# Kernel optimization log

Hardware: AMD Instinct MI355X
Metric: run time of the kernel (lower is better)

The kernel has to match this reference:

```python
import jax, jax.numpy as jnp
import numpy as np

SCALE = 0.0625      # spatial_scale
OUT = 7             # out_size (== part_size)
C_OUT = 256         # output_dim (== input channels, group_size=1)
SPP = 4             # sample_per_part
TRANS_STD = 0.1
FC_DIM = 1024
B, H, W = 4, 128, 128
N_ROI = 2000
IMG = 2048.0        # H / SCALE


def _round_half(x):
    # CUDA round(): half away from zero (coords are non-negative here)
    return jnp.floor(x + 0.5)


def deform_roi_pool(data, rois, offset):
    """Faithful port of deform_roi_pooling (DCNv2 deform PS-ROI pooling, group_size=1).
    data: [B,C,H,W]; rois: [N,5]; offset: None or [N,2,OUT,OUT]. Returns [N,C,OUT,OUT]."""
    Bn, C, Hh, Ww = data.shape
    N = rois.shape[0]
    b = rois[:, 0].astype(jnp.int32)
    sw = _round_half(rois[:, 1]) * SCALE - 0.5
    sh = _round_half(rois[:, 2]) * SCALE - 0.5
    ew = (_round_half(rois[:, 3]) + 1.0) * SCALE - 0.5
    eh = (_round_half(rois[:, 4]) + 1.0) * SCALE - 0.5
    rw = jnp.maximum(ew - sw, 0.1)
    rh = jnp.maximum(eh - sh, 0.1)
    bw, bh = rw / OUT, rh / OUT              # bin sizes
    subw, subh = bw / SPP, bh / SPP          # sub-bin sizes

    ph, pw = jnp.meshgrid(jnp.arange(OUT, dtype=data.dtype),
                          jnp.arange(OUT, dtype=data.dtype), indexing='ij')
    wstart = pw[None] * bw[:, None, None] + sw[:, None, None]   # [N,OUT,OUT]
    hstart = ph[None] * bh[:, None, None] + sh[:, None, None]
    if offset is not None:
        # part_size == out_size -> part index == bin index
        wstart = wstart + offset[:, 0] * TRANS_STD * rw[:, None, None]
        hstart = hstart + offset[:, 1] * TRANS_STD * rh[:, None, None]

    ih2, iw2 = jnp.meshgrid(jnp.arange(SPP, dtype=data.dtype),
                            jnp.arange(SPP, dtype=data.dtype), indexing='ij')
    ih2, iw2 = ih2.reshape(-1), iw2.reshape(-1)  # [SPP*SPP]
    # sample coords [S2, N, OUT, OUT]
    ws = wstart[None] + iw2[:, None, None, None] * subw[None, :, None, None]
    hs = hstart[None] + ih2[:, None, None, None] * subh[None, :, None, None]

    bb = b[:, None, None]  # [N,1,1]

    def body(carry, coords):
        acc, cnt = carry
        w, h = coords                                 # [N,OUT,OUT]
        valid = (w >= -0.5) & (w <= Ww - 0.5) & (h >= -0.5) & (h <= Hh - 0.5)
        wc = jnp.clip(w, 0.0, Ww - 1.0)
        hc = jnp.clip(h, 0.0, Hh - 1.0)
        x0 = jnp.floor(wc).astype(jnp.int32)
        y0 = jnp.floor(hc).astype(jnp.int32)
        x1 = jnp.minimum(x0 + 1, Ww - 1)
        y1 = jnp.minimum(y0 + 1, Hh - 1)
        dx = wc - x0
        dy = hc - y0
        v00 = data[bb, :, y0, x0]   # [N,OUT,OUT,C]
        v01 = data[bb, :, y0, x1]
        v10 = data[bb, :, y1, x0]
        v11 = data[bb, :, y1, x1]
        val = (((1 - dx) * (1 - dy))[..., None] * v00
               + (dx * (1 - dy))[..., None] * v01
               + ((1 - dx) * dy)[..., None] * v10
               + (dx * dy)[..., None] * v11)
        val = jnp.where(valid[..., None], val, 0.0)
        return (acc + val, cnt + valid.astype(data.dtype)), None

    init = (jnp.zeros((N, OUT, OUT, C), data.dtype),
            jnp.zeros((N, OUT, OUT), data.dtype))
    (s, cnt), _ = jax.lax.scan(body, init, (ws, hs))
    out = jnp.where(cnt[..., None] > 0, s / jnp.maximum(cnt, 1.0)[..., None], 0.0)
    return jnp.transpose(out, (0, 3, 1, 2))  # [N,C,OUT,OUT]


def setup_inputs() -> dict:
    key = jax.random.key(0)
    ks = jax.random.split(key, 16)
    data = jax.random.normal(ks[0], (B, C_OUT, H, W), dtype=jnp.float32)
    bidx = jax.random.randint(ks[1], (N_ROI,), 0, B).astype(jnp.float32)
    x1 = jax.random.uniform(ks[2], (N_ROI,), minval=0.0, maxval=IMG - 64.0)
    y1 = jax.random.uniform(ks[3], (N_ROI,), minval=0.0, maxval=IMG - 64.0)
    wbox = jax.random.uniform(ks[4], (N_ROI,), minval=16.0, maxval=400.0)
    hbox = jax.random.uniform(ks[5], (N_ROI,), minval=16.0, maxval=400.0)
    rois = jnp.stack([bidx, x1, y1,
                      jnp.minimum(x1 + wbox, IMG - 1.0),
                      jnp.minimum(y1 + hbox, IMG - 1.0)], axis=1)
    fin = OUT * OUT * C_OUT  # 12544
    def lin(k, i, o, s=None):
        s = (1.0 / np.sqrt(i)) if s is None else s
        return jax.random.normal(k, (i, o), dtype=jnp.float32) * s
    return {
        'data': data, 'rois': rois,
        'w1': lin(ks[6], fin, FC_DIM), 'b1': jnp.zeros((FC_DIM,), jnp.float32),
        'w2': lin(ks[7], FC_DIM, FC_DIM), 'b2': jnp.zeros((FC_DIM,), jnp.float32),
        'w3': lin(ks[8], FC_DIM, OUT * OUT * 2, 0.01), 'b3': jnp.zeros((OUT * OUT * 2,), jnp.float32),
        'mw1': lin(ks[9], fin, FC_DIM), 'mb1': jnp.zeros((FC_DIM,), jnp.float32),
        'mw2': lin(ks[10], FC_DIM, OUT * OUT, 0.01), 'mb2': jnp.zeros((OUT * OUT,), jnp.float32),
    }


def reference(data, rois, w1, b1, w2, b2, w3, b3, mw1, mb1, mw2, mb2):
    n = rois.shape[0]
    x = deform_roi_pool(data, rois, None)              # [N,C,OUT,OUT]
    xf = x.reshape(n, -1)
    h = jax.nn.relu(xf @ w1 + b1)
    h = jax.nn.relu(h @ w2 + b2)
    offset = (h @ w3 + b3).reshape(n, 2, OUT, OUT)
    m = jax.nn.relu(xf @ mw1 + mb1)
    mask = jax.nn.sigmoid(m @ mw2 + mb2).reshape(n, 1, OUT, OUT)
    feat = deform_roi_pool(data, rois, offset) * mask
    return feat
```

## Files before the change

### kernel.cpp

```cpp
#include <hip/hip_runtime.h>
#include <math.h>

#define WDIM 128
#define HDIM 128
#define BDIM 4
#define CDIM 256
#define NROI 2000
#define MPAD 2048
#define FIN  12544
#define FC   1024
#define HWC  (HDIM * WDIM * CDIM)

typedef unsigned short bf16r;
typedef unsigned short u16;
typedef __attribute__((ext_vector_type(8))) short bf16x8;
typedef __attribute__((ext_vector_type(4))) float f32x4;
typedef __attribute__((ext_vector_type(8))) _Float16 half8;
typedef __attribute__((ext_vector_type(8))) unsigned short ushort8v;

__device__ __forceinline__ bf16r f2bf(float f) {
    unsigned u = __float_as_uint(f);
    u += 0x7FFFu + ((u >> 16) & 1u);
    return (bf16r)(u >> 16);
}
__device__ __forceinline__ u16 f2h(float f) {
    union { u16 s; _Float16 h; } c; c.h = (_Float16)f; return c.s;
}

__device__ __forceinline__ void async16(const bf16r* g, bf16r* l) {
    __builtin_amdgcn_global_load_lds(
        (const __attribute__((address_space(1))) unsigned int*)g,
        (__attribute__((address_space(3))) unsigned int*)l, 16, 0, 0);
}

#define VMW(n) asm volatile("s_waitcnt vmcnt(" #n ")" ::: "memory")
#define BARRIER() __builtin_amdgcn_s_barrier()

__device__ __forceinline__ void roi_geom(const float* __restrict__ rois, int n,
                                         int& b, float& sw, float& sh,
                                         float& rw, float& rh) {
    const float* r = rois + (size_t)n * 5;
    b = (int)r[0];
    float r1 = floorf(r[1] + 0.5f);
    float r2 = floorf(r[2] + 0.5f);
    float r3 = floorf(r[3] + 0.5f);
    float r4 = floorf(r[4] + 0.5f);
    sw = r1 * 0.0625f - 0.5f;
    sh = r2 * 0.0625f - 0.5f;
    float ew = (r3 + 1.0f) * 0.0625f - 0.5f;
    float eh = (r4 + 1.0f) * 0.0625f - 0.5f;
    rw = fmaxf(ew - sw, 0.1f);
    rh = fmaxf(eh - sh, 0.1f);
}

__device__ __forceinline__ void build_geometry(
        int n, int tid, const float* __restrict__ rois,
        const float* __restrict__ offs,
        const float* __restrict__ maskb,
        float* axW, unsigned* axMeta, uint2* wpix, int* npx, float* scale) {
    if (tid < 98) {
        int po = tid >> 1, axis = tid & 1;
        int b; float sw, sh, rw, rh;
        roi_geom(rois, n, b, sw, sh, rw, rh);
        float bw = rw * (1.f / 7.f), bh = rh * (1.f / 7.f);
        int ph = po / 7, pw = po - ph * 7;
        float start, sub;
        if (axis == 0) {
            start = (float)pw * bw + sw;
            if (offs) start += offs[(size_t)n * 98 + po] * 0.1f * rw;
            sub = bw * 0.25f;
        } else {
            start = (float)ph * bh + sh;
            if (offs) start += offs[(size_t)n * 98 + 49 + po] * 0.1f * rh;
            sub = bh * 0.25f;
        }
        float wsl[5] = {0.f, 0.f, 0.f, 0.f, 0.f};
        int base = 0, cnt = 0, mx = 0, any = 0;
#pragma unroll
        for (int i = 0; i < 4; ++i) {
            float p = start + (float)i * sub;
            bool valid = (p >= -0.5f) & (p <= 127.5f);
            float pc = fminf(fmaxf(p, 0.f), 127.f);
            int p0 = (int)floorf(pc);
            float d = pc - (float)p0;
            int p1 = min(p0 + 1, 127);
            if (valid) {
                if (!any) { base = p0; any = 1; }
                int c0 = p0 - base, c1 = p1 - base;
                float w0 = 1.f - d;
#pragma unroll
                for (int k = 0; k < 5; ++k)
                    wsl[k] += ((c0 == k) ? w0 : 0.f) + ((c1 == k) ? d : 0.f);
                cnt++;
                mx = max(mx, c1);
            }
        }
        int N = any ? mx + 1 : 0;
        axMeta[tid] = (unsigned)(N | (cnt << 3) | (base << 6));
#pragma unroll
        for (int k = 0; k < 5; ++k) axW[tid * 5 + k] = wsl[k];
    }
    __syncthreads();
    if (tid < 245) {
        int po = tid / 5, r = tid - po * 5;
        unsigned mx_ = axMeta[po * 2], my_ = axMeta[po * 2 + 1];
        int NX = mx_ & 7, NY = my_ & 7;
        int bx = (mx_ >> 6) & 127, by = (my_ >> 6) & 127;
        if (r == 0) {
            int cntx = (mx_ >> 3) & 7, cnty = (my_ >> 3) & 7;
            int ct = cntx * cnty;
            float sc = (ct > 0) ? 1.f / (float)ct : 0.f;
            if (maskb) sc *= (ct > 0) ? maskb[(size_t)n * 49 + po] : 0.f;
            npx[po] = NX * NY;
            scale[po] = sc;
        }
        if (r < NY) {
            float wyr = axW[(po * 2 + 1) * 5 + r];
            unsigned rowoff = (unsigned)(((by + r) * 128 + bx) * 512);
#pragma unroll
            for (int c = 0; c < 5; ++c)
                if (c < NX)
                    wpix[po * 28 + r * NX + c] =
                        make_uint2(rowoff + (unsigned)c * 512u,
                                   __float_as_uint(wyr * axW[po * 2 * 5 + c]));
        }
    }
    __syncthreads();
}

__global__ __launch_bounds__(256) void transpose_kernel(const float* __restrict__ data,
                                                        u16* __restrict__ data_t) {
    __shared__ float t[32][33];
    int x0 = blockIdx.x << 5;
    int c0 = blockIdx.y << 5;
    int b  = blockIdx.z >> 7;
    int y  = blockIdx.z & 127;
    int tx = threadIdx.x, ty = threadIdx.y;
#pragma unroll
    for (int i = 0; i < 32; i += 8)
        t[ty + i][tx] = data[(((size_t)b * CDIM + c0 + ty + i) * HDIM + y) * WDIM + x0 + tx];
    __syncthreads();
#pragma unroll
    for (int i = 0; i < 32; i += 8)
        data_t[(((size_t)b * HDIM + y) * WDIM + x0 + ty + i) * CDIM + c0 + tx] = f2h(t[tx][ty + i]);
}

__global__ __launch_bounds__(256) void conv_kernel(const float* __restrict__ srcA,
                                                   const float* __restrict__ srcB,
                                                   int nsplit, int ncols, int Nout,
                                                   int K, int perm,
                                                   bf16r* __restrict__ dst) {
    __shared__ float t[32][33];
    int k0 = blockIdx.x << 5, n0 = blockIdx.y << 5;
    int tx = threadIdx.x & 31, ty = threadIdx.x >> 5;
#pragma unroll
    for (int i = 0; i < 32; i += 8) {
        int k = k0 + ty + i;
        int n = n0 + tx;
        const float* s = (n < nsplit) ? srcA : srcB;
        int col = (n < nsplit) ? n : n - nsplit;
        int row = perm ? ((k & 255) * 49 + (k >> 8)) : k;
        float v = (n < Nout && col < ncols) ? s[(size_t)row * ncols + col] : 0.f;
        t[ty + i][tx] = v;
    }
    __syncthreads();
#pragma unroll
    for (int i = 0; i < 32; i += 8) {
        int n = n0 + ty + i;
        if (n < Nout) dst[(size_t)n * K + k0 + tx] = f2bf(t[tx][ty + i]);
    }
}

__global__ __launch_bounds__(512) void pool1_kernel(const u16* __restrict__ data_t,
                                                    const float* __restrict__ rois,
                                                    bf16r* __restrict__ xf) {
    __shared__ ushort tileX[49][264];
    __shared__ float axW[98 * 5];
    __shared__ unsigned axMeta[98];
    __shared__ uint2 wpix[49 * 28];
    __shared__ int npx[49];
    __shared__ float scale[49];
    int n = blockIdx.x, tid = threadIdx.x;
    build_geometry(n, tid, rois, nullptr, nullptr, axW, axMeta, wpix, npx, scale);
    int b = (int)rois[(size_t)n * 5];
    int wave = tid >> 6, lane = tid & 63, shalf = lane >> 5, c8 = (lane & 31) << 3;
    const char* dpb = (const char*)(data_t + (size_t)b * HWC + c8);
    for (int po = wave * 2 + shalf; po < 49; po += 16) {
        int npe = npx[po];
        float sc = scale[po];
        const uint2* wp = wpix + po * 28;
        float a[8];
#pragma unroll
        for (int k = 0; k < 8; ++k) a[k] = 0.f;
        int p = 0;
        for (; p + 2 <= npe; p += 2) {
            uint2 q0 = wp[p], q1 = wp[p + 1];
            half8 v0 = *(const half8*)(dpb + q0.x);
            half8 v1 = *(const half8*)(dpb + q1.x);
            float w0 = __uint_as_float(q0.y), w1 = __uint_as_float(q1.y);
#pragma unroll
            for (int k = 0; k < 8; ++k) a[k] += w0 * (float)v0[k];
#pragma unroll
            for (int k = 0; k < 8; ++k) a[k] += w1 * (float)v1[k];
        }
        if (p < npe) {
            uint2 q0 = wp[p];
            half8 v0 = *(const half8*)(dpb + q0.x);
            float w0 = __uint_as_float(q0.y);
#pragma unroll
            for (int k = 0; k < 8; ++k) a[k] += w0 * (float)v0[k];
        }
        ushort8v o;
#pragma unroll
        for (int k = 0; k < 8; ++k) o[k] = f2bf(a[k] * sc);
        *(ushort8v*)&tileX[po][c8] = o;
    }
    __syncthreads();
    bf16r* xp = xf + (size_t)n * FIN;
    for (int u = tid; u < 3136; u += 512) {
        int k0 = u << 2;
        ushort4 o;
#pragma unroll
        for (int j = 0; j < 4; ++j) {
            int k = k0 + j;
            int c = k / 49;
            int po = k - c * 49;
            ((ushort*)&o)[j] = tileX[po][c];
        }
        *(ushort4*)(xp + k0) = o;
    }
}

__global__ __launch_bounds__(512) void pool2_kernel(const u16* __restrict__ data_t,
                                                    const float* __restrict__ rois,
                                                    const float* __restrict__ offs,
                                                    const float* __restrict__ maskb,
                                                    float* __restrict__ out) {
    __shared__ float tile[49 * 128];
    __shared__ float axW[98 * 5];
    __shared__ unsigned axMeta[98];
    __shared__ uint2 wpix[49 * 28];
    __shared__ int npx[49];
    __shared__ float scale[49];
    int n = blockIdx.x, chalf = blockIdx.y, tid = threadIdx.x;
    build_geometry(n, tid, rois, offs, maskb, axW, axMeta, wpix, npx, scale);
    int b = (int)rois[(size_t)n * 5];
    int wave = tid >> 6, lane = tid & 63, q = lane >> 4, c8 = (lane & 15) << 3;
    const char* dpb = (const char*)(data_t + (size_t)b * HWC + chalf * 128 + c8);
    for (int po = wave * 4 + q; po < 49; po += 32) {
        int npe = npx[po];
        float sc = scale[po];
        const uint2* wp = wpix + po * 28;
        float a[8];
#pragma unroll
        for (int k = 0; k < 8; ++k) a[k] = 0.f;
        int p = 0;
        for (; p + 2 <= npe; p += 2) {
            uint2 q0 = wp[p], q1 = wp[p + 1];
            half8 v0 = *(const half8*)(dpb + q0.x);
            half8 v1 = *(const half8*)(dpb + q1.x);
            float w0 = __uint_as_float(q0.y), w1 = __uint_as_float(q1.y);
#pragma unroll
            for (int k = 0; k < 8; ++k) a[k] += w0 * (float)v0[k];
#pragma unroll
            for (int k = 0; k < 8; ++k) a[k] += w1 * (float)v1[k];
        }
        if (p < npe) {
            uint2 q0 = wp[p];
            half8 v0 = *(const half8*)(dpb + q0.x);
            float w0 = __uint_as_float(q0.y);
#pragma unroll
            for (int k = 0; k < 8; ++k) a[k] += w0 * (float)v0[k];
        }
        int cs = c8 ^ ((po & 7) << 3);
        float4 lo = make_float4(a[0] * sc, a[1] * sc, a[2] * sc, a[3] * sc);
        float4 hi = make_float4(a[4] * sc, a[5] * sc, a[6] * sc, a[7] * sc);
        *(float4*)&tile[po * 128 + cs] = lo;
        *(float4*)&tile[po * 128 + cs + 4] = hi;
    }
    __syncthreads();
    float* op = out + (size_t)n * FIN + (size_t)chalf * 6272;
    for (int i = tid; i < 6272; i += 512) {
        int c = i / 49, po = i - c * 49;
        op[i] = tile[po * 128 + (c ^ ((po & 7) << 3))];
    }
}

#define STAGE_A(buf, h, kt) do { \
    async16(Abase + (size_t)(kt) * 64 + sAoff[h][0], &lds[buf][0][((h) * 128 + wave * 8) * 64]); \
    async16(Abase + (size_t)(kt) * 64 + sAoff[h][1], &lds[buf][0][((h) * 128 + 64 + wave * 8) * 64]); \
} while (0)
#define STAGE_B(buf, h, kt) do { \
    async16(Bbase + (size_t)(kt) * 64 + sBoff[h][0], &lds[buf][1][((h) * 128 + wave * 8) * 64]); \
    async16(Bbase + (size_t)(kt) * 64 + sBoff[h][1], &lds[buf][1][((h) * 128 + 64 + wave * 8) * 64]); \
} while (0)
#define LDA_HALF(buf, mh) do { \
    const char* Ar = (const char*)&lds[buf][0][0] + aQ + (mh) * 16384; \
    _Pragma("unroll") for (int i = 0; i < 4; ++i) \
        _Pragma("unroll") for (int ks = 0; ks < 2; ++ks) \
            aF[i][ks] = *(const bf16x8*)(Ar + i * 2048 + fRB[ks]); \
} while (0)
#define LDB_HALF(dst, buf, nh) do { \
    const char* Br = (const char*)&lds[buf][1][0] + bQ + (nh) * 16384; \
    _Pragma("unroll") for (int jf = 0; jf < 2; ++jf) \
        _Pragma("unroll") for (int ks = 0; ks < 2; ++ks) \
            dst[jf][ks] = *(const bf16x8*)(Br + jf * 2048 + fRB[ks]); \
} while (0)
#define MMA_Q(mh, nh, B) do { \
    __builtin_amdgcn_s_setprio(1); \
    _Pragma("unroll") for (int i = 0; i < 4; ++i) \
        _Pragma("unroll") for (int jf = 0; jf < 2; ++jf) \
            _Pragma("unroll") for (int ks = 0; ks < 2; ++ks) \
                acc[(mh) * 4 + i][(nh) * 2 + jf] = __builtin_amdgcn_mfma_f32_16x16x32_bf16( \
                    aF[i][ks], B[jf][ks], acc[(mh) * 4 + i][(nh) * 2 + jf], 0, 0, 0); \
    __builtin_amdgcn_s_setprio(0); \
} while (0)

__global__ __launch_bounds__(512, 2) void gemm256_kernel(
        const bf16r* __restrict__ A, int lda,
        const bf16r* __restrict__ Bt, int ldb,
        float* __restrict__ P, int Npad, int KS, int ktiles) {
    __shared__ bf16r lds[2][2][256 * 64];
    int tid = threadIdx.x;
    int wave = tid >> 6, lane = tid & 63;
    int l15 = lane & 15, quad = lane >> 4;
    int wm = wave >> 2, wn = wave & 3;

    int idx = blockIdx.x + gridDim.x * blockIdx.y;
    int nid = (idx & 7) * ((gridDim.x * gridDim.y) >> 3) + (idx >> 3);
    int bx = nid % gridDim.x, by = nid / gridDim.x;
    int m0 = by << 8, n0 = bx << 8;
    int z = blockIdx.z;

    int sAoff[2][2], sBoff[2][2];
#pragma unroll
    for (int h = 0; h < 2; ++h)
#pragma unroll
        for (int j = 0; j < 2; ++j) {
            int slot = h * 128 + j * 64 + wave * 8 + (lane >> 3);
            int g = (lane & 7) ^ ((slot >> 1) & 7);
            int rowA = ((slot >> 6) & 1) * 128 + (slot >> 7) * 64 + (slot & 63);
            int colB = ((slot >> 5) & 3) * 64 + (slot >> 7) * 32 + (slot & 31);
            sAoff[h][j] = rowA * lda + g * 8;
            sBoff[h][j] = colB * ldb + g * 8;
        }
    const bf16r* Abase = A + (size_t)m0 * lda;
    const bf16r* Bbase = Bt + (size_t)n0 * ldb;

    int fRB[2];
#pragma unroll
    for (int ks = 0; ks < 2; ++ks)
        fRB[ks] = l15 * 128 + ((((ks << 2) + quad) ^ ((l15 >> 1) & 7)) << 4);
    int aQ = wm * 8192;
    int bQ = wn * 4096;

    f32x4 acc[8][4];
#pragma unroll
    for (int i = 0; i < 8; ++i)
#pragma unroll
        for (int j = 0; j < 4; ++j) acc[i][j] = (f32x4){0.f, 0.f, 0.f, 0.f};
    bf16x8 aF[4][2], bF0[2][2], bF1[2][2];

    int tb = ((ktiles * z) / KS) & ~1;
    int te = (z == KS - 1) ? ktiles : ((ktiles * (z + 1)) / KS) & ~1;
    int nit = (te - tb) >> 1;

    STAGE_A(0, 0, tb); STAGE_B(0, 0, tb); STAGE_A(0, 1, tb); STAGE_B(0, 1, tb);
    STAGE_A(1, 0, tb + 1); STAGE_B(1, 0, tb + 1);
    VMW(4);
    BARRIER();

    for (int it = 0; it < nit; ++it) {
        int t1 = tb + 2 * it + 1, nx0 = t1 + 1, nx1 = t1 + 2;
        bool last = (it == nit - 1);
        LDA_HALF(0, 0); LDB_HALF(bF0, 0, 0);
        STAGE_A(1, 1, t1);
        BARRIER();
        MMA_Q(0, 0, bF0);
        BARRIER();

        LDB_HALF(bF1, 0, 1);
        STAGE_B(1, 1, t1);
        BARRIER();
        MMA_Q(0, 1, bF1);
        BARRIER();

        LDA_HALF(0, 1);
        if (!last) STAGE_A(0, 0, nx0);
        BARRIER();
        MMA_Q(1, 1, bF1);
        BARRIER();

        if (!last) STAGE_B(0, 0, nx0);
        BARRIER();
        MMA_Q(1, 0, bF0);
        if (last) { VMW(0); } else { VMW(4); }
        BARRIER();

        LDA_HALF(1, 0); LDB_HALF(bF0, 1, 0);
        if (!last) STAGE_A(0, 1, nx0);
        BARRIER();
        MMA_Q(0, 0, bF0);
        BARRIER();

        LDB_HALF(bF1, 1, 1);
        if (!last) STAGE_B(0, 1, nx0);
        BARRIER();
        MMA_Q(0, 1, bF1);
        BARRIER();

        LDA_HALF(1, 1);
        if (!last) STAGE_A(1, 0, nx1);
        BARRIER();
        MMA_Q(1, 1, bF1);
        BARRIER();

        if (!last) STAGE_B(1, 0, nx1);
        BARRIER();
        MMA_Q(1, 0, bF0);
        if (!last) { VMW(4); }
        BARRIER();
    }

    float* Pp = P + (size_t)z * MPAD * Npad;
#pragma unroll
    for (int I = 0; I < 8; ++I) {
        int row = m0 + wm * 128 + I * 16 + quad * 4;
#pragma unroll
        for (int J = 0; J < 4; ++J) {
            int col = n0 + wn * 64 + J * 16 + l15;
            float* o = Pp + (size_t)row * Npad + col;
#pragma unroll
            for (int r = 0; r < 4; ++r) o[(size_t)r * Npad] = acc[I][J][r];
        }
    }
}

__global__ __launch_bounds__(256) void gemm_mfma_kernel(
        const bf16r* __restrict__ A, int lda,
        const bf16r* __restrict__ Bt, int K,
        float* __restrict__ P, int Npad, int KS) {
    __shared__ bf16r As[128 * 32];
    __shared__ bf16r Bs[128 * 32];
    int tid = threadIdx.x;
    int wave = tid >> 6, lane = tid & 63;
    int nwgxy = gridDim.x * gridDim.y;
    int idx = blockIdx.x + gridDim.x * blockIdx.y;
    int chunk = nwgxy >> 3;
    int nid = (idx & 7) * chunk + (idx >> 3);
    int bx = nid % gridDim.x, by = nid / gridDim.x;
    int m0 = by << 7, n0 = bx << 7;
    int z = blockIdx.z;

    int srow = lane >> 2;
    int kchunk = ((lane & 3) ^ ((lane >> 3) & 3)) << 3;
    const bf16r* aG0 = A + (size_t)(m0 + wave * 32 + srow) * lda + kchunk;
    const bf16r* aG1 = A + (size_t)(m0 + wave * 32 + 16 + srow) * lda + kchunk;
    const bf16r* bG0 = Bt + (size_t)(n0 + wave * 32 + srow) * K + kchunk;
    const bf16r* bG1 = Bt + (size_t)(n0 + wave * 32 + 16 + srow) * K + kchunk;
    bf16r* aL0 = As + wave * 1024;
    bf16r* aL1 = As + wave * 1024 + 512;
    bf16r* bL0 = Bs + wave * 1024;
    bf16r* bL1 = Bs + wave * 1024 + 512;

    int l15 = lane & 15, quad = lane >> 4;
    int wr = wave >> 1, wc = wave & 1;
    int psw = (quad ^ ((l15 >> 1) & 3)) << 3;
    int aoff[4], boff[4];
#pragma unroll
    for (int t = 0; t < 4; ++t) {
        aoff[t] = ((wr * 64 + t * 16 + l15) * 32 + psw) * 2;
        boff[t] = ((wc * 64 + t * 16 + l15) * 32 + psw) * 2;
    }

    f32x4 acc[4][4];
#pragma unroll
    for (int i = 0; i < 4; ++i)
#pragma unroll
        for (int j = 0; j < 4; ++j) acc[i][j] = (f32x4){0.f, 0.f, 0.f, 0.f};

    int iters = K >> 5;
    int i0 = (int)((long)iters * z / KS);
    int i1 = (int)((long)iters * (z + 1) / KS);

    {
        size_t k0 = (size_t)i0 << 5;
        async16(aG0 + k0, aL0); async16(aG1 + k0, aL1);
        async16(bG0 + k0, bL0); async16(bG1 + k0, bL1);
    }
    for (int it = i0; it < i1; ++it) {
        __syncthreads();
        bf16x8 af[4], bfv[4];
#pragma unroll
        for (int t = 0; t < 4; ++t) af[t] = *(const bf16x8*)((const char*)As + aoff[t]);
#pragma unroll
        for (int t = 0; t < 4; ++t) bfv[t] = *(const bf16x8*)((const char*)Bs + boff[t]);
        __syncthreads();
        if (it + 1 < i1) {
            size_t k0 = (size_t)(it + 1) << 5;
            async16(aG0 + k0, aL0); async16(aG1 + k0, aL1);
            async16(bG0 + k0, bL0); async16(bG1 + k0, bL1);
        }
#pragma unroll
        for (int i = 0; i < 4; ++i)
#pragma unroll
            for (int j = 0; j < 4; ++j)
                acc[i][j] = __builtin_amdgcn_mfma_f32_16x16x32_bf16(af[i], bfv[j], acc[i][j], 0, 0, 0);
    }

    float* Pp = P + (size_t)z * MPAD * Npad;
#pragma unroll
    for (int i = 0; i < 4; ++i) {
        int row = m0 + wr * 64 + i * 16 + quad * 4;
#pragma unroll
        for (int j = 0; j < 4; ++j) {
            int col = n0 + wc * 64 + j * 16 + l15;
            float* o = Pp + (size_t)row * Npad + col;
#pragma unroll
            for (int r = 0; r < 4; ++r) o[(size_t)r * Npad] = acc[i][j][r];
        }
    }
}

__global__ __launch_bounds__(256) void reduce_kernel(
        const float* __restrict__ P, int shift, int KS,
        const float* __restrict__ bias0, const float* __restrict__ bias1, int bsplit,
        void* __restrict__ Out, int ldo, int M, int Nreal, int outmode) {
    int idx = (blockIdx.x * 256 + threadIdx.x) << 2;
    int Npad = 1 << shift;
    int row = idx >> shift, col = idx & (Npad - 1);
    f32x4 s = (f32x4){0.f, 0.f, 0.f, 0.f};
    size_t plane = (size_t)MPAD << shift;
    for (int zz = 0; zz < KS; ++zz) s += *(const f32x4*)(P + (size_t)zz * plane + idx);
    if (row < M) {
#pragma unroll
        for (int e = 0; e < 4; ++e) {
            int c = col + e;
            if (c < Nreal) {
                float b = (c < bsplit) ? bias0[c] : bias1[c - bsplit];
                float v = s[e] + b;
                if (outmode == 0) {
                    v = fmaxf(v, 0.f);
                    ((bf16r*)Out)[(size_t)row * ldo + c] = f2bf(v);
                } else {
                    if (outmode == 2) v = 1.f / (1.f + expf(-v));
                    ((float*)Out)[(size_t)row * ldo + c] = v;
                }
            }
        }
    }
}

extern "C" void kernel_launch(void* const* d_in, const int* in_sizes, int n_in,
                              void* d_out, int out_size, void* d_ws, size_t ws_size,
                              hipStream_t stream) {
    const float* data = (const float*)d_in[0];
    const float* rois = (const float*)d_in[1];
    const float* w1   = (const float*)d_in[2];
    const float* b1   = (const float*)d_in[3];
    const float* w2   = (const float*)d_in[4];
    const float* b2   = (const float*)d_in[5];
    const float* w3   = (const float*)d_in[6];
    const float* b3   = (const float*)d_in[7];
    const float* mw1  = (const float*)d_in[8];
    const float* mb1  = (const float*)d_in[9];
    const float* mw2  = (const float*)d_in[10];
    const float* mb2  = (const float*)d_in[11];
    float* out = (float*)d_out;

    char* w = (char*)d_ws;
    size_t off = 0;
    auto carve = [&](size_t bytes) {
        void* p = w + off;
        off += (bytes + 255) & ~(size_t)255;
        return p;
    };
    u16* data_t   = (u16*)carve((size_t)BDIM * HDIM * WDIM * CDIM * 2);
    bf16r* xf     = (bf16r*)carve((size_t)MPAD * FIN * 2);
    bf16r* bt1    = (bf16r*)carve((size_t)MPAD * FIN * 2);
    bf16r* hm     = (bf16r*)carve((size_t)MPAD * 2048 * 2);
    bf16r* h2     = (bf16r*)carve((size_t)MPAD * 1024 * 2);
    bf16r* bt2    = (bf16r*)carve((size_t)1024 * 1024 * 2);
    bf16r* bt3    = (bf16r*)carve((size_t)128 * 1024 * 2);
    bf16r* bt4    = (bf16r*)carve((size_t)128 * 1024 * 2);
    float* offs   = (float*)carve((size_t)NROI * 98 * 4);
    float* maskb  = (float*)carve((size_t)NROI * 49 * 4);
    float* P      = (float*)(w + off);
    size_t plane  = (size_t)MPAD * 2048 * 4;
    size_t avail  = (ws_size > off) ? ws_size - off : 0;
    int use256 = (avail >= 4 * plane);

    conv_kernel<<<dim3(392, 64), 256, 0, stream>>>(w1, mw1, 1024, 1024, 2048, FIN, 0, bt1);
    conv_kernel<<<dim3(32, 32), 256, 0, stream>>>(w2, w2, 1 << 30, 1024, 1024, 1024, 0, bt2);
    conv_kernel<<<dim3(32, 4), 256, 0, stream>>>(w3, w3, 1 << 30, 98, 98, 1024, 0, bt3);
    conv_kernel<<<dim3(32, 2), 256, 0, stream>>>(mw2, mw2, 1 << 30, 49, 49, 1024, 0, bt4);
    transpose_kernel<<<dim3(4, 8, 512), dim3(32, 8), 0, stream>>>(data, data_t);
    pool1_kernel<<<dim3(NROI), 512, 0, stream>>>(data_t, rois, xf);

    if (use256) {
        gemm256_kernel<<<dim3(8, 8, 4), 512, 0, stream>>>(xf, FIN, bt1, FIN, P, 2048, 4, 196);
        reduce_kernel<<<4096, 256, 0, stream>>>(P, 11, 4, b1, mb1, 1024, hm, 2048, NROI, 2048, 0);
        gemm256_kernel<<<dim3(4, 8, 8), 512, 0, stream>>>(hm, 2048, bt2, 1024, P, 1024, 8, 16);
        reduce_kernel<<<2048, 256, 0, stream>>>(P, 10, 8, b2, b2, 1 << 30, h2, 1024, NROI, 1024, 0);
    } else {
        gemm_mfma_kernel<<<dim3(16, 16, 3), 256, 0, stream>>>(xf, FIN, bt1, FIN, P, 2048, 3);
        reduce_kernel<<<4096, 256, 0, stream>>>(P, 11, 3, b1, mb1, 1024, hm, 2048, NROI, 2048, 0);
        gemm_mfma_kernel<<<dim3(8, 16, 4), 256, 0, stream>>>(hm, 2048, bt2, 1024, P, 1024, 4);
        reduce_kernel<<<2048, 256, 0, stream>>>(P, 10, 4, b2, b2, 1 << 30, h2, 1024, NROI, 1024, 0);
    }
    gemm_mfma_kernel<<<dim3(1, 16, 8), 256, 0, stream>>>(h2, 1024, bt3, 1024, P, 128, 8);
    reduce_kernel<<<256, 256, 0, stream>>>(P, 7, 8, b3, b3, 1 << 30, offs, 98, NROI, 98, 1);
    gemm_mfma_kernel<<<dim3(1, 16, 8), 256, 0, stream>>>(hm + 1024, 2048, bt4, 1024, P, 128, 8);
    reduce_kernel<<<256, 256, 0, stream>>>(P, 7, 8, mb2, mb2, 1 << 30, maskb, 49, NROI, 49, 2);

    pool2_kernel<<<dim3(NROI, 2), 512, 0, stream>>>(data_t, rois, offs, maskb, out);
}
```

Measured before the change: 526.9 us.

## Reorder ROI blocks by batch index and use 128-tile GEMM for second FC

Adds a single-block kernel that builds a remap of ROIs grouped by batch image. Both pooling kernels then process ROIs in that order, so blocks running at the same time read the same image plane and get better L2 reuse. The second FC layer now always uses the 128-tile MFMA GEMM with split-K of 4 instead of the 256-tile variant. The remap kernel adds one small serial launch, and its atomic ordering inside a batch is nondeterministic, though outputs are written by ROI index and stay correct.

```diff
diff --git a/kernel.cpp b/kernel.cpp
--- a/kernel.cpp
+++ b/kernel.cpp
@@ -51,6 +51,27 @@
     float eh = (r4 + 1.0f) * 0.0625f - 0.5f;
     rw = fmaxf(ew - sw, 0.1f);
     rh = fmaxf(eh - sh, 0.1f);
+}
+
+__global__ __launch_bounds__(256) void order_kernel(const float* __restrict__ rois,
+                                                    int* __restrict__ remap) {
+    __shared__ int cnt[4], base[4];
+    int tid = threadIdx.x;
+    if (tid < 4) cnt[tid] = 0;
+    __syncthreads();
+    for (int n = tid; n < NROI; n += 256)
+        atomicAdd(&cnt[(int)rois[(size_t)n * 5]], 1);
+    __syncthreads();
+    if (tid == 0) {
+        int s = 0;
+        for (int i = 0; i < 4; ++i) { base[i] = s; s += cnt[i]; cnt[i] = 0; }
+    }
+    __syncthreads();
+    for (int n = tid; n < NROI; n += 256) {
+        int b = (int)rois[(size_t)n * 5];
+        int pos = base[b] + atomicAdd(&cnt[b], 1);
+        remap[pos] = n;
+    }
 }
 
 __device__ __forceinline__ void build_geometry(
@@ -173,6 +194,7 @@
 
 __global__ __launch_bounds__(512) void pool1_kernel(const u16* __restrict__ data_t,
                                                     const float* __restrict__ rois,
+                                                    const int* __restrict__ remap,
                                                     bf16r* __restrict__ xf) {
     __shared__ ushort tileX[49][264];
     __shared__ float axW[98 * 5];
@@ -180,7 +202,7 @@
     __shared__ uint2 wpix[49 * 28];
     __shared__ int npx[49];
     __shared__ float scale[49];
-    int n = blockIdx.x, tid = threadIdx.x;
+    int n = remap[blockIdx.x], tid = threadIdx.x;
     build_geometry(n, tid, rois, nullptr, nullptr, axW, axMeta, wpix, npx, scale);
     int b = (int)rois[(size_t)n * 5];
     int wave = tid >> 6, lane = tid & 63, shalf = lane >> 5, c8 = (lane & 31) << 3;
@@ -233,6 +255,7 @@
 
 __global__ __launch_bounds__(512) void pool2_kernel(const u16* __restrict__ data_t,
                                                     const float* __restrict__ rois,
+                                                    const int* __restrict__ remap,
                                                     const float* __restrict__ offs,
                                                     const float* __restrict__ maskb,
                                                     float* __restrict__ out) {
@@ -242,7 +265,7 @@
     __shared__ uint2 wpix[49 * 28];
     __shared__ int npx[49];
     __shared__ float scale[49];
-    int n = blockIdx.x, chalf = blockIdx.y, tid = threadIdx.x;
+    int n = remap[blockIdx.x], chalf = blockIdx.y, tid = threadIdx.x;
     build_geometry(n, tid, rois, offs, maskb, axW, axMeta, wpix, npx, scale);
     int b = (int)rois[(size_t)n * 5];
     int wave = tid >> 6, lane = tid & 63, q = lane >> 4, c8 = (lane & 15) << 3;
@@ -585,33 +608,33 @@
     bf16r* bt4    = (bf16r*)carve((size_t)128 * 1024 * 2);
     float* offs   = (float*)carve((size_t)NROI * 98 * 4);
     float* maskb  = (float*)carve((size_t)NROI * 49 * 4);
+    int*   remap  = (int*)carve((size_t)NROI * 4);
     float* P      = (float*)(w + off);
     size_t plane  = (size_t)MPAD * 2048 * 4;
     size_t avail  = (ws_size > off) ? ws_size - off : 0;
     int use256 = (avail >= 4 * plane);
 
+    order_kernel<<<1, 256, 0, stream>>>(rois, remap);
     conv_kernel<<<dim3(392, 64), 256, 0, stream>>>(w1, mw1, 1024, 1024, 2048, FIN, 0, bt1);
     conv_kernel<<<dim3(32, 32), 256, 0, stream>>>(w2, w2, 1 << 30, 1024, 1024, 1024, 0, bt2);
     conv_kernel<<<dim3(32, 4), 256, 0, stream>>>(w3, w3, 1 << 30, 98, 98, 1024, 0, bt3);
     conv_kernel<<<dim3(32, 2), 256, 0, stream>>>(mw2, mw2, 1 << 30, 49, 49, 1024, 0, bt4);
     transpose_kernel<<<dim3(4, 8, 512), dim3(32, 8), 0, stream>>>(data, data_t);
-    pool1_kernel<<<dim3(NROI), 512, 0, stream>>>(data_t, rois, xf);
+    pool1_kernel<<<dim3(NROI), 512, 0, stream>>>(data_t, rois, remap, xf);
 
     if (use256) {
         gemm256_kernel<<<dim3(8, 8, 4), 512, 0, stream>>>(xf, FIN, bt1, FIN, P, 2048, 4, 196);
         reduce_kernel<<<4096, 256, 0, stream>>>(P, 11, 4, b1, mb1, 1024, hm, 2048, NROI, 2048, 0);
-        gemm256_kernel<<<dim3(4, 8, 8), 512, 0, stream>>>(hm, 2048, bt2, 1024, P, 1024, 8, 16);
-        reduce_kernel<<<2048, 256, 0, stream>>>(P, 10, 8, b2, b2, 1 << 30, h2, 1024, NROI, 1024, 0);
     } else {
         gemm_mfma_kernel<<<dim3(16, 16, 3), 256, 0, stream>>>(xf, FIN, bt1, FIN, P, 2048, 3);
         reduce_kernel<<<4096, 256, 0, stream>>>(P, 11, 3, b1, mb1, 1024, hm, 2048, NROI, 2048, 0);
-        gemm_mfma_kernel<<<dim3(8, 16, 4), 256, 0, stream>>>(hm, 2048, bt2, 1024, P, 1024, 4);
-        reduce_kernel<<<2048, 256, 0, stream>>>(P, 10, 4, b2, b2, 1 << 30, h2, 1024, NROI, 1024, 0);
-    }
+    }
+    gemm_mfma_kernel<<<dim3(8, 16, 4), 256, 0, stream>>>(hm, 2048, bt2, 1024, P, 1024, 4);
+    reduce_kernel<<<2048, 256, 0, stream>>>(P, 10, 4, b2, b2, 1 << 30, h2, 1024, NROI, 1024, 0);
     gemm_mfma_kernel<<<dim3(1, 16, 8), 256, 0, stream>>>(h2, 1024, bt3, 1024, P, 128, 8);
     reduce_kernel<<<256, 256, 0, stream>>>(P, 7, 8, b3, b3, 1 << 30, offs, 98, NROI, 98, 1);
     gemm_mfma_kernel<<<dim3(1, 16, 8), 256, 0, stream>>>(hm + 1024, 2048, bt4, 1024, P, 128, 8);
     reduce_kernel<<<256, 256, 0, stream>>>(P, 7, 8, mb2, mb2, 1 << 30, maskb, 49, NROI, 49, 2);
 
-    pool2_kernel<<<dim3(NROI, 2), 512, 0, stream>>>(data_t, rois, offs, maskb, out);
-}
+    pool2_kernel<<<dim3(NROI, 2), 512, 0, stream>>>(data_t, rois, remap, offs, maskb, out);
+}
```

Measured after the change: 521.8 us. No clear change (-1.0%).
